# Kernel tuning notes

Measured on AMD Instinct MI355X. Metric: run time of the kernel, lower is better.

The kernel has to match this reference:

```python
import jax, jax.numpy as jnp
import numpy as np

E = 8      # num_experts
K = 2      # active_experts
D = 1024   # embed_size
H = 4 * D  # ffn hidden


def setup_inputs() -> dict:
    key = jax.random.key(0)
    ks = jax.random.split(key, 7)
    s_in = 1.0 / np.sqrt(D)
    s_h = 1.0 / np.sqrt(H)
    return {
        "x":  jax.random.normal(ks[0], (4, 2048, D), dtype=jnp.float32),
        "Wr": jax.random.uniform(ks[1], (D, E), jnp.float32, -s_in, s_in),
        "br": jax.random.uniform(ks[2], (E,), jnp.float32, -s_in, s_in),
        "W1": jax.random.uniform(ks[3], (E, D, H), jnp.float32, -s_in, s_in),
        "b1": jax.random.uniform(ks[4], (E, H), jnp.float32, -s_in, s_in),
        "W2": jax.random.uniform(ks[5], (E, H, D), jnp.float32, -s_h, s_h),
        "b2": jax.random.uniform(ks[6], (E, D), jnp.float32, -s_h, s_h),
    }


def reference(x, Wr, br, W1, b1, W2, b2):
    # Router: softmax over experts, top-k values, renormalize.
    logits = jnp.einsum("bsd,de->bse", x, Wr) + br            # [B,S,E]
    probs = jax.nn.softmax(logits, axis=-1)
    topk_vals, _ = jax.lax.top_k(probs, K)                     # [B,S,K]
    gates = topk_vals / topk_vals.sum(axis=-1, keepdims=True)  # [B,S,K]

    # Original bug (reproduced faithfully): the mask-multiply-sum is identity,
    # and slot index i selects experts[i], so only experts 0..K-1 run on ALL tokens.
    h = jax.nn.relu(jnp.einsum("bsd,kdh->bskh", x, W1[:K]) + b1[:K])  # [B,S,K,H]
    y = jnp.einsum("bskh,khd->bskd", h, W2[:K]) + b2[:K]               # [B,S,K,D]
    return jnp.einsum("bskd,bsk->bsd", y, gates)                       # [B,S,D]
```

## Files before the change

kernel.cpp:

```cpp
#include <hip/hip_runtime.h>
#include <hip/hip_bf16.h>

#define T_TOK 8192
#define DDIM  1024
#define HDIM  4096
#define KCAT  8192
#define NE    8

typedef __attribute__((ext_vector_type(8))) __bf16 bf16x8;
typedef __attribute__((ext_vector_type(4))) float  f32x4;

__device__ __forceinline__ unsigned short f2bf(float f) {
  union { float f; unsigned u; } v; v.f = f;
  unsigned r = v.u + 0x7fffu + ((v.u >> 16) & 1u);
  return (unsigned short)(r >> 16);
}

__device__ __forceinline__ void gl_lds16(const unsigned short* g, char* l) {
  __builtin_amdgcn_global_load_lds(
      (__attribute__((address_space(1))) const void*)g,
      (__attribute__((address_space(3))) void*)l,
      16, 0, 0);
}

__global__ __launch_bounds__(256) void k_router(
    const float* __restrict__ x, const float* __restrict__ Wr,
    const float* __restrict__ br, unsigned short* __restrict__ xb,
    float* __restrict__ gates)
{
  const int lane = threadIdx.x & 63;
  const int wv   = threadIdx.x >> 6;
  const int t    = blockIdx.x * 4 + wv;
  const float* xr = x + (size_t)t * DDIM;
  unsigned short* xo = xb + (size_t)t * DDIM;

  float acc[NE];
#pragma unroll
  for (int e = 0; e < NE; ++e) acc[e] = 0.f;

#pragma unroll
  for (int i = 0; i < 4; ++i) {
    float4 v = *(const float4*)(xr + i * 256 + lane * 4);
    ushort4 o;
    o.x = f2bf(v.x); o.y = f2bf(v.y); o.z = f2bf(v.z); o.w = f2bf(v.w);
    *(ushort4*)(xo + i * 256 + lane * 4) = o;
    float vs[4] = {v.x, v.y, v.z, v.w};
#pragma unroll
    for (int j = 0; j < 4; ++j) {
      const float4* wr = (const float4*)(Wr + (size_t)(i * 256 + lane * 4 + j) * NE);
      float4 w0 = wr[0], w1 = wr[1];
      acc[0] += vs[j] * w0.x; acc[1] += vs[j] * w0.y;
      acc[2] += vs[j] * w0.z; acc[3] += vs[j] * w0.w;
      acc[4] += vs[j] * w1.x; acc[5] += vs[j] * w1.y;
      acc[6] += vs[j] * w1.z; acc[7] += vs[j] * w1.w;
    }
  }
#pragma unroll
  for (int e = 0; e < NE; ++e) {
#pragma unroll
    for (int s = 32; s > 0; s >>= 1) acc[e] += __shfl_xor(acc[e], s, 64);
  }
  if (lane == 0) {
    float lg[NE];
#pragma unroll
    for (int e = 0; e < NE; ++e) lg[e] = acc[e] + br[e];
    int a1 = 0; float m1 = lg[0];
#pragma unroll
    for (int e = 1; e < NE; ++e) if (lg[e] > m1) { m1 = lg[e]; a1 = e; }
    float m2 = -3.4e38f;
#pragma unroll
    for (int e = 0; e < NE; ++e) if (e != a1 && lg[e] > m2) m2 = lg[e];
    float g0 = 1.f / (1.f + expf(m2 - m1));
    gates[t * 2 + 0] = g0;
    gates[t * 2 + 1] = 1.f - g0;
  }
}

__global__ __launch_bounds__(256) void k_transpose(
    const float* __restrict__ in, unsigned short* __restrict__ out,
    int R, int C, int S, size_t inz, size_t outz)
{
  __shared__ float tile[32][33];
  in  += (size_t)blockIdx.z * inz;
  out += (size_t)blockIdx.z * outz;
  const int c0 = blockIdx.x * 32, r0 = blockIdx.y * 32;
  const int tx = threadIdx.x & 31, ty = threadIdx.x >> 5;
#pragma unroll
  for (int i = 0; i < 32; i += 8)
    tile[ty + i][tx] = in[(size_t)(r0 + ty + i) * C + (c0 + tx)];
  __syncthreads();
#pragma unroll
  for (int i = 0; i < 32; i += 8)
    out[(size_t)(c0 + ty + i) * S + (r0 + tx)] = f2bf(tile[tx][ty + i]);
}

template<int NT, int MODE>
__global__ __launch_bounds__(512, 2) void k_gemm2(
    const unsigned short* __restrict__ A,
    const unsigned short* __restrict__ B,
    unsigned short* __restrict__ Hout,
    float* __restrict__ P0, float* __restrict__ P1,
    const float* __restrict__ bias,
    const float* __restrict__ gates,
    int KA, int KB)
{
  __shared__ __align__(16) char lds[2 * 32768];

  const int tid = threadIdx.x;
  const int l = tid & 63, g = (l >> 4), l15 = l & 15;
  const int w = tid >> 6;
  const int wm = w >> 2, wn = w & 3;

  int bmIdx, bnIdx, bzIdx;
  {
    int lin = ((blockIdx.z * gridDim.y) + blockIdx.y) * gridDim.x + blockIdx.x;
    int xcd = lin & 7, slot = (lin >> 3) & 31;
    if (MODE == 0) {
      int r = lin >> 8;
      bmIdx = r * 8 + (slot >> 2);
      bnIdx = xcd * 4 + (slot & 3);
      bzIdx = 0;
    } else {
      bzIdx = xcd & 1;
      bmIdx = (xcd >> 1) * 8 + (slot >> 2);
      bnIdx = slot & 3;
    }
  }
  const int bn = bnIdx * 256;
  const int bm = bmIdx * 256;
  const int koff = bzIdx * (NT * 32);

  const int srow = tid >> 2;
  const int sc = (tid & 3) ^ ((srow >> 1) & 3);
  const unsigned short* As = A + (size_t)(bm + srow) * KA + koff + sc * 8;
  const unsigned short* Bs = B + (size_t)(bn + srow) * KB + koff + sc * 8;

  auto stage = [&](int T, int reg) {
    const unsigned short* src = (reg ? Bs : As) + T * 32;
    size_t rstride = (size_t)128 * (reg ? KB : KA);
    char* dst = lds + ((T & 1) << 15) + (reg << 14) + tid * 16;
    gl_lds16(src, dst);
    gl_lds16(src + rstride, dst + 8192);
  };

  int aoff[2][4], boff[4];
#pragma unroll
  for (int mh = 0; mh < 2; ++mh)
#pragma unroll
    for (int mi = 0; mi < 4; ++mi) {
      int r = wm * 128 + mh * 64 + mi * 16 + l15;
      aoff[mh][mi] = r * 64 + ((g ^ ((r >> 1) & 3)) * 16);
    }
#pragma unroll
  for (int nj = 0; nj < 4; ++nj) {
    int r = wn * 64 + nj * 16 + l15;
    boff[nj] = r * 64 + ((g ^ ((r >> 1) & 3)) * 16);
  }

  f32x4 acc[8][4];
#pragma unroll
  for (int i = 0; i < 8; ++i)
#pragma unroll
    for (int j = 0; j < 4; ++j) acc[i][j] = (f32x4){0.f, 0.f, 0.f, 0.f};

  stage(0, 0); stage(0, 1);

#define MFMA16(AI, A0, A1, A2, A3)                                                     \
    acc[(AI)+0][0] = __builtin_amdgcn_mfma_f32_16x16x32_bf16(A0, vb0, acc[(AI)+0][0], 0,0,0); \
    acc[(AI)+0][1] = __builtin_amdgcn_mfma_f32_16x16x32_bf16(A0, vb1, acc[(AI)+0][1], 0,0,0); \
    acc[(AI)+0][2] = __builtin_amdgcn_mfma_f32_16x16x32_bf16(A0, vb2, acc[(AI)+0][2], 0,0,0); \
    acc[(AI)+0][3] = __builtin_amdgcn_mfma_f32_16x16x32_bf16(A0, vb3, acc[(AI)+0][3], 0,0,0); \
    acc[(AI)+1][0] = __builtin_amdgcn_mfma_f32_16x16x32_bf16(A1, vb0, acc[(AI)+1][0], 0,0,0); \
    acc[(AI)+1][1] = __builtin_amdgcn_mfma_f32_16x16x32_bf16(A1, vb1, acc[(AI)+1][1], 0,0,0); \
    acc[(AI)+1][2] = __builtin_amdgcn_mfma_f32_16x16x32_bf16(A1, vb2, acc[(AI)+1][2], 0,0,0); \
    acc[(AI)+1][3] = __builtin_amdgcn_mfma_f32_16x16x32_bf16(A1, vb3, acc[(AI)+1][3], 0,0,0); \
    acc[(AI)+2][0] = __builtin_amdgcn_mfma_f32_16x16x32_bf16(A2, vb0, acc[(AI)+2][0], 0,0,0); \
    acc[(AI)+2][1] = __builtin_amdgcn_mfma_f32_16x16x32_bf16(A2, vb1, acc[(AI)+2][1], 0,0,0); \
    acc[(AI)+2][2] = __builtin_amdgcn_mfma_f32_16x16x32_bf16(A2, vb2, acc[(AI)+2][2], 0,0,0); \
    acc[(AI)+2][3] = __builtin_amdgcn_mfma_f32_16x16x32_bf16(A2, vb3, acc[(AI)+2][3], 0,0,0); \
    acc[(AI)+3][0] = __builtin_amdgcn_mfma_f32_16x16x32_bf16(A3, vb0, acc[(AI)+3][0], 0,0,0); \
    acc[(AI)+3][1] = __builtin_amdgcn_mfma_f32_16x16x32_bf16(A3, vb1, acc[(AI)+3][1], 0,0,0); \
    acc[(AI)+3][2] = __builtin_amdgcn_mfma_f32_16x16x32_bf16(A3, vb2, acc[(AI)+3][2], 0,0,0); \
    acc[(AI)+3][3] = __builtin_amdgcn_mfma_f32_16x16x32_bf16(A3, vb3, acc[(AI)+3][3], 0,0,0);

#define MPH(BUF, STG) do {                                                     \
    asm volatile("s_waitcnt vmcnt(0)" ::: "memory");                           \
    __builtin_amdgcn_s_barrier();                                              \
    const char* Ar_ = lds + ((BUF) << 15);                                     \
    const char* Br_ = Ar_ + 16384;                                             \
    bf16x8 vb0 = *(const bf16x8*)(Br_ + boff[0]);                              \
    bf16x8 vb1 = *(const bf16x8*)(Br_ + boff[1]);                              \
    bf16x8 vb2 = *(const bf16x8*)(Br_ + boff[2]);                              \
    bf16x8 vb3 = *(const bf16x8*)(Br_ + boff[3]);                              \
    bf16x8 vc0 = *(const bf16x8*)(Ar_ + aoff[0][0]);                           \
    bf16x8 vc1 = *(const bf16x8*)(Ar_ + aoff[0][1]);                           \
    bf16x8 vc2 = *(const bf16x8*)(Ar_ + aoff[0][2]);                           \
    bf16x8 vc3 = *(const bf16x8*)(Ar_ + aoff[0][3]);                           \
    bf16x8 vn0 = *(const bf16x8*)(Ar_ + aoff[1][0]);                           \
    bf16x8 vn1 = *(const bf16x8*)(Ar_ + aoff[1][1]);                           \
    bf16x8 vn2 = *(const bf16x8*)(Ar_ + aoff[1][2]);                           \
    bf16x8 vn3 = *(const bf16x8*)(Ar_ + aoff[1][3]);                           \
    asm volatile("" ::: "memory");                                             \
    STG;                                                                       \
    __builtin_amdgcn_s_setprio(1);                                             \
    MFMA16(0, vc0, vc1, vc2, vc3)                                              \
    MFMA16(4, vn0, vn1, vn2, vn3)                                              \
    __builtin_amdgcn_s_setprio(0);                                             \
    __builtin_amdgcn_s_barrier();                                              \
  } while (0)

  for (int tt = 0; tt < NT / 2 - 1; ++tt) {
    int t2 = tt * 2;
    MPH(0, { stage(t2 + 1, 0); stage(t2 + 1, 1); });
    MPH(1, { stage(t2 + 2, 0); stage(t2 + 2, 1); });
  }
  MPH(0, { stage(NT - 1, 0); stage(NT - 1, 1); });
  MPH(1, ;);
#undef MPH
#undef MFMA16

  if constexpr (MODE == 0) {
    const int ge = bn >> 12;
    float bcol[4];
#pragma unroll
    for (int nj = 0; nj < 4; ++nj) bcol[nj] = bias[bn + wn * 64 + nj * 16 + l15];
#pragma unroll
    for (int mi = 0; mi < 8; ++mi) {
#pragma unroll
      for (int rr = 0; rr < 4; ++rr) {
        int row = bm + wm * 128 + mi * 16 + g * 4 + rr;
        float gate = gates[row * 2 + ge];
        size_t rb = (size_t)row * KCAT + bn + wn * 64 + l15;
#pragma unroll
        for (int nj = 0; nj < 4; ++nj) {
          float v = acc[mi][nj][rr] + bcol[nj];
          Hout[rb + nj * 16] = f2bf(fmaxf(v, 0.f) * gate);
        }
      }
    }
  } else {
    float* P = bzIdx ? P1 : P0;
#pragma unroll
    for (int mi = 0; mi < 8; ++mi) {
#pragma unroll
      for (int rr = 0; rr < 4; ++rr) {
        int row = bm + wm * 128 + mi * 16 + g * 4 + rr;
        size_t rb = (size_t)row * DDIM + bn + wn * 64 + l15;
#pragma unroll
        for (int nj = 0; nj < 4; ++nj) P[rb + nj * 16] = acc[mi][nj][rr];
      }
    }
  }
}

__global__ __launch_bounds__(256) void k_combine(
    const float* __restrict__ P1, const float* __restrict__ b2,
    const float* __restrict__ gates, float* __restrict__ O)
{
  size_t i = ((size_t)blockIdx.x * 256 + threadIdx.x) * 4;
  int row = (int)(i >> 10), d = (int)(i & 1023);
  float g0 = gates[row * 2], g1 = gates[row * 2 + 1];
  float4 p0 = *(const float4*)(O + i);
  float4 p1 = *(const float4*)(P1 + i);
  float4 ba = *(const float4*)(b2 + d);
  float4 bb = *(const float4*)(b2 + DDIM + d);
  float4 r;
  r.x = p0.x + p1.x + g0 * ba.x + g1 * bb.x;
  r.y = p0.y + p1.y + g0 * ba.y + g1 * bb.y;
  r.z = p0.z + p1.z + g0 * ba.z + g1 * bb.z;
  r.w = p0.w + p1.w + g0 * ba.w + g1 * bb.w;
  *(float4*)(O + i) = r;
}

extern "C" void kernel_launch(void* const* d_in, const int* in_sizes, int n_in,
                              void* d_out, int out_size, void* d_ws, size_t ws_size,
                              hipStream_t stream) {
  const float* x  = (const float*)d_in[0];
  const float* Wr = (const float*)d_in[1];
  const float* br = (const float*)d_in[2];
  const float* W1 = (const float*)d_in[3];
  const float* b1 = (const float*)d_in[4];
  const float* W2 = (const float*)d_in[5];
  const float* b2 = (const float*)d_in[6];

  char* ws = (char*)d_ws;
  unsigned short* xb    = (unsigned short*)(ws);
  unsigned short* W1T   = (unsigned short*)(ws + (16u << 20));
  unsigned short* W2T   = (unsigned short*)(ws + (32u << 20));
  float*          gates = (float*)(ws + (48u << 20));
  unsigned short* hbuf  = (unsigned short*)(ws + (49u << 20));
  float*          P1    = (float*)(ws);

  k_router<<<dim3(T_TOK / 4), dim3(256), 0, stream>>>(x, Wr, br, xb, gates);

  k_transpose<<<dim3(HDIM / 32, DDIM / 32, 2), dim3(256), 0, stream>>>(
      W1, W1T, DDIM, HDIM, DDIM, (size_t)DDIM * HDIM, (size_t)HDIM * DDIM);
  k_transpose<<<dim3(DDIM / 32, HDIM / 32, 2), dim3(256), 0, stream>>>(
      W2, W2T, HDIM, DDIM, KCAT, (size_t)HDIM * DDIM, (size_t)HDIM);

  k_gemm2<32, 0><<<dim3(KCAT / 256, T_TOK / 256, 1), dim3(512), 0, stream>>>(
      xb, W1T, hbuf, nullptr, nullptr, b1, gates, DDIM, DDIM);

  k_gemm2<128, 1><<<dim3(DDIM / 256, T_TOK / 256, 2), dim3(512), 0, stream>>>(
      hbuf, W2T, nullptr, (float*)d_out, P1, nullptr, nullptr, KCAT, KCAT);

  k_combine<<<dim3(T_TOK * DDIM / 4 / 256), dim3(256), 0, stream>>>(
      P1, b2, gates, (float*)d_out);
}
```

Baseline: 325.4 us.

## Software-pipeline LDS fragment reads with double register buffers in GEMM main loop

Restructures the GEMM main loop so that LDS fragment reads for the next k-tile go into a second register set while MFMAs consume the current one. This removes one barrier per phase and lets LDS read latency overlap with matrix math. The launch bound's min-blocks-per-CU hint is dropped, since the doubled fragment registers raise VGPR pressure, which may lower occupancy. A sched_barrier pins the instruction order.

Result: no change. 322.0 us (-1.0%).

```diff
diff --git a/kernel.cpp b/kernel.cpp
--- a/kernel.cpp
+++ b/kernel.cpp
@@ -95,7 +95,7 @@
 }
 
 template<int NT, int MODE>
-__global__ __launch_bounds__(512, 2) void k_gemm2(
+__global__ __launch_bounds__(512) void k_gemmp(
     const unsigned short* __restrict__ A,
     const unsigned short* __restrict__ B,
     unsigned short* __restrict__ Hout,
@@ -163,61 +163,88 @@
 #pragma unroll
     for (int j = 0; j < 4; ++j) acc[i][j] = (f32x4){0.f, 0.f, 0.f, 0.f};
 
-  stage(0, 0); stage(0, 1);
-
-#define MFMA16(AI, A0, A1, A2, A3)                                                     \
-    acc[(AI)+0][0] = __builtin_amdgcn_mfma_f32_16x16x32_bf16(A0, vb0, acc[(AI)+0][0], 0,0,0); \
-    acc[(AI)+0][1] = __builtin_amdgcn_mfma_f32_16x16x32_bf16(A0, vb1, acc[(AI)+0][1], 0,0,0); \
-    acc[(AI)+0][2] = __builtin_amdgcn_mfma_f32_16x16x32_bf16(A0, vb2, acc[(AI)+0][2], 0,0,0); \
-    acc[(AI)+0][3] = __builtin_amdgcn_mfma_f32_16x16x32_bf16(A0, vb3, acc[(AI)+0][3], 0,0,0); \
-    acc[(AI)+1][0] = __builtin_amdgcn_mfma_f32_16x16x32_bf16(A1, vb0, acc[(AI)+1][0], 0,0,0); \
-    acc[(AI)+1][1] = __builtin_amdgcn_mfma_f32_16x16x32_bf16(A1, vb1, acc[(AI)+1][1], 0,0,0); \
-    acc[(AI)+1][2] = __builtin_amdgcn_mfma_f32_16x16x32_bf16(A1, vb2, acc[(AI)+1][2], 0,0,0); \
-    acc[(AI)+1][3] = __builtin_amdgcn_mfma_f32_16x16x32_bf16(A1, vb3, acc[(AI)+1][3], 0,0,0); \
-    acc[(AI)+2][0] = __builtin_amdgcn_mfma_f32_16x16x32_bf16(A2, vb0, acc[(AI)+2][0], 0,0,0); \
-    acc[(AI)+2][1] = __builtin_amdgcn_mfma_f32_16x16x32_bf16(A2, vb1, acc[(AI)+2][1], 0,0,0); \
-    acc[(AI)+2][2] = __builtin_amdgcn_mfma_f32_16x16x32_bf16(A2, vb2, acc[(AI)+2][2], 0,0,0); \
-    acc[(AI)+2][3] = __builtin_amdgcn_mfma_f32_16x16x32_bf16(A2, vb3, acc[(AI)+2][3], 0,0,0); \
-    acc[(AI)+3][0] = __builtin_amdgcn_mfma_f32_16x16x32_bf16(A3, vb0, acc[(AI)+3][0], 0,0,0); \
-    acc[(AI)+3][1] = __builtin_amdgcn_mfma_f32_16x16x32_bf16(A3, vb1, acc[(AI)+3][1], 0,0,0); \
-    acc[(AI)+3][2] = __builtin_amdgcn_mfma_f32_16x16x32_bf16(A3, vb2, acc[(AI)+3][2], 0,0,0); \
-    acc[(AI)+3][3] = __builtin_amdgcn_mfma_f32_16x16x32_bf16(A3, vb3, acc[(AI)+3][3], 0,0,0);
-
-#define MPH(BUF, STG) do {                                                     \
+  bf16x8 RA[12], RB[12];
+
+#define READS(R, b) do {                                                       \
+    const char* Ar_ = lds + ((b) << 15);                                       \
+    const char* Br_ = Ar_ + 16384;                                             \
+    R[0]  = *(const bf16x8*)(Br_ + boff[0]);                                   \
+    R[1]  = *(const bf16x8*)(Br_ + boff[1]);                                   \
+    R[2]  = *(const bf16x8*)(Br_ + boff[2]);                                   \
+    R[3]  = *(const bf16x8*)(Br_ + boff[3]);                                   \
+    R[4]  = *(const bf16x8*)(Ar_ + aoff[0][0]);                                \
+    R[5]  = *(const bf16x8*)(Ar_ + aoff[0][1]);                                \
+    R[6]  = *(const bf16x8*)(Ar_ + aoff[0][2]);                                \
+    R[7]  = *(const bf16x8*)(Ar_ + aoff[0][3]);                                \
+    R[8]  = *(const bf16x8*)(Ar_ + aoff[1][0]);                                \
+    R[9]  = *(const bf16x8*)(Ar_ + aoff[1][1]);                                \
+    R[10] = *(const bf16x8*)(Ar_ + aoff[1][2]);                                \
+    R[11] = *(const bf16x8*)(Ar_ + aoff[1][3]);                                \
+  } while (0)
+
+#define MFMA32(R)                                                              \
+    acc[0][0] = __builtin_amdgcn_mfma_f32_16x16x32_bf16(R[4],  R[0], acc[0][0], 0,0,0); \
+    acc[0][1] = __builtin_amdgcn_mfma_f32_16x16x32_bf16(R[4],  R[1], acc[0][1], 0,0,0); \
+    acc[0][2] = __builtin_amdgcn_mfma_f32_16x16x32_bf16(R[4],  R[2], acc[0][2], 0,0,0); \
+    acc[0][3] = __builtin_amdgcn_mfma_f32_16x16x32_bf16(R[4],  R[3], acc[0][3], 0,0,0); \
+    acc[1][0] = __builtin_amdgcn_mfma_f32_16x16x32_bf16(R[5],  R[0], acc[1][0], 0,0,0); \
+    acc[1][1] = __builtin_amdgcn_mfma_f32_16x16x32_bf16(R[5],  R[1], acc[1][1], 0,0,0); \
+    acc[1][2] = __builtin_amdgcn_mfma_f32_16x16x32_bf16(R[5],  R[2], acc[1][2], 0,0,0); \
+    acc[1][3] = __builtin_amdgcn_mfma_f32_16x16x32_bf16(R[5],  R[3], acc[1][3], 0,0,0); \
+    acc[2][0] = __builtin_amdgcn_mfma_f32_16x16x32_bf16(R[6],  R[0], acc[2][0], 0,0,0); \
+    acc[2][1] = __builtin_amdgcn_mfma_f32_16x16x32_bf16(R[6],  R[1], acc[2][1], 0,0,0); \
+    acc[2][2] = __builtin_amdgcn_mfma_f32_16x16x32_bf16(R[6],  R[2], acc[2][2], 0,0,0); \
+    acc[2][3] = __builtin_amdgcn_mfma_f32_16x16x32_bf16(R[6],  R[3], acc[2][3], 0,0,0); \
+    acc[3][0] = __builtin_amdgcn_mfma_f32_16x16x32_bf16(R[7],  R[0], acc[3][0], 0,0,0); \
+    acc[3][1] = __builtin_amdgcn_mfma_f32_16x16x32_bf16(R[7],  R[1], acc[3][1], 0,0,0); \
+    acc[3][2] = __builtin_amdgcn_mfma_f32_16x16x32_bf16(R[7],  R[2], acc[3][2], 0,0,0); \
+    acc[3][3] = __builtin_amdgcn_mfma_f32_16x16x32_bf16(R[7],  R[3], acc[3][3], 0,0,0); \
+    acc[4][0] = __builtin_amdgcn_mfma_f32_16x16x32_bf16(R[8],  R[0], acc[4][0], 0,0,0); \
+    acc[4][1] = __builtin_amdgcn_mfma_f32_16x16x32_bf16(R[8],  R[1], acc[4][1], 0,0,0); \
+    acc[4][2] = __builtin_amdgcn_mfma_f32_16x16x32_bf16(R[8],  R[2], acc[4][2], 0,0,0); \
+    acc[4][3] = __builtin_amdgcn_mfma_f32_16x16x32_bf16(R[8],  R[3], acc[4][3], 0,0,0); \
+    acc[5][0] = __builtin_amdgcn_mfma_f32_16x16x32_bf16(R[9],  R[0], acc[5][0], 0,0,0); \
+    acc[5][1] = __builtin_amdgcn_mfma_f32_16x16x32_bf16(R[9],  R[1], acc[5][1], 0,0,0); \
+    acc[5][2] = __builtin_amdgcn_mfma_f32_16x16x32_bf16(R[9],  R[2], acc[5][2], 0,0,0); \
+    acc[5][3] = __builtin_amdgcn_mfma_f32_16x16x32_bf16(R[9],  R[3], acc[5][3], 0,0,0); \
+    acc[6][0] = __builtin_amdgcn_mfma_f32_16x16x32_bf16(R[10], R[0], acc[6][0], 0,0,0); \
+    acc[6][1] = __builtin_amdgcn_mfma_f32_16x16x32_bf16(R[10], R[1], acc[6][1], 0,0,0); \
+    acc[6][2] = __builtin_amdgcn_mfma_f32_16x16x32_bf16(R[10], R[2], acc[6][2], 0,0,0); \
+    acc[6][3] = __builtin_amdgcn_mfma_f32_16x16x32_bf16(R[10], R[3], acc[6][3], 0,0,0); \
+    acc[7][0] = __builtin_amdgcn_mfma_f32_16x16x32_bf16(R[11], R[0], acc[7][0], 0,0,0); \
+    acc[7][1] = __builtin_amdgcn_mfma_f32_16x16x32_bf16(R[11], R[1], acc[7][1], 0,0,0); \
+    acc[7][2] = __builtin_amdgcn_mfma_f32_16x16x32_bf16(R[11], R[2], acc[7][2], 0,0,0); \
+    acc[7][3] = __builtin_amdgcn_mfma_f32_16x16x32_bf16(R[11], R[3], acc[7][3], 0,0,0);
+
+#define PH(RD, RDB, MF, DOSTG, STGT) do {                                      \
     asm volatile("s_waitcnt vmcnt(0)" ::: "memory");                           \
     __builtin_amdgcn_s_barrier();                                              \
-    const char* Ar_ = lds + ((BUF) << 15);                                     \
-    const char* Br_ = Ar_ + 16384;                                             \
-    bf16x8 vb0 = *(const bf16x8*)(Br_ + boff[0]);                              \
-    bf16x8 vb1 = *(const bf16x8*)(Br_ + boff[1]);                              \
-    bf16x8 vb2 = *(const bf16x8*)(Br_ + boff[2]);                              \
-    bf16x8 vb3 = *(const bf16x8*)(Br_ + boff[3]);                              \
-    bf16x8 vc0 = *(const bf16x8*)(Ar_ + aoff[0][0]);                           \
-    bf16x8 vc1 = *(const bf16x8*)(Ar_ + aoff[0][1]);                           \
-    bf16x8 vc2 = *(const bf16x8*)(Ar_ + aoff[0][2]);                           \
-    bf16x8 vc3 = *(const bf16x8*)(Ar_ + aoff[0][3]);                           \
-    bf16x8 vn0 = *(const bf16x8*)(Ar_ + aoff[1][0]);                           \
-    bf16x8 vn1 = *(const bf16x8*)(Ar_ + aoff[1][1]);                           \
-    bf16x8 vn2 = *(const bf16x8*)(Ar_ + aoff[1][2]);                           \
-    bf16x8 vn3 = *(const bf16x8*)(Ar_ + aoff[1][3]);                           \
+    READS(RD, RDB);                                                            \
+    if (DOSTG) { stage((STGT), 0); stage((STGT), 1); }                         \
     asm volatile("" ::: "memory");                                             \
-    STG;                                                                       \
+    __builtin_amdgcn_sched_barrier(0);                                         \
     __builtin_amdgcn_s_setprio(1);                                             \
-    MFMA16(0, vc0, vc1, vc2, vc3)                                              \
-    MFMA16(4, vn0, vn1, vn2, vn3)                                              \
+    MFMA32(MF)                                                                 \
     __builtin_amdgcn_s_setprio(0);                                             \
-    __builtin_amdgcn_s_barrier();                                              \
   } while (0)
 
+  stage(0, 0); stage(0, 1);
+  asm volatile("s_waitcnt vmcnt(0)" ::: "memory");
+  __builtin_amdgcn_s_barrier();
+  READS(RA, 0);
+  stage(1, 0); stage(1, 1);
+
   for (int tt = 0; tt < NT / 2 - 1; ++tt) {
-    int t2 = tt * 2;
-    MPH(0, { stage(t2 + 1, 0); stage(t2 + 1, 1); });
-    MPH(1, { stage(t2 + 2, 0); stage(t2 + 2, 1); });
-  }
-  MPH(0, { stage(NT - 1, 0); stage(NT - 1, 1); });
-  MPH(1, ;);
-#undef MPH
-#undef MFMA16
+    PH(RB, 1, RA, true, 2 * tt + 2);
+    PH(RA, 0, RB, true, 2 * tt + 3);
+  }
+  PH(RB, 1, RA, false, 0);
+  __builtin_amdgcn_s_setprio(1);
+  MFMA32(RB)
+  __builtin_amdgcn_s_setprio(0);
+#undef PH
+#undef MFMA32
+#undef READS
 
   if constexpr (MODE == 0) {
     const int ge = bn >> 12;
@@ -298,10 +325,10 @@
   k_transpose<<<dim3(DDIM / 32, HDIM / 32, 2), dim3(256), 0, stream>>>(
       W2, W2T, HDIM, DDIM, KCAT, (size_t)HDIM * DDIM, (size_t)HDIM);
 
-  k_gemm2<32, 0><<<dim3(KCAT / 256, T_TOK / 256, 1), dim3(512), 0, stream>>>(
+  k_gemmp<32, 0><<<dim3(KCAT / 256, T_TOK / 256, 1), dim3(512), 0, stream>>>(
       xb, W1T, hbuf, nullptr, nullptr, b1, gates, DDIM, DDIM);
 
-  k_gemm2<128, 1><<<dim3(DDIM / 256, T_TOK / 256, 2), dim3(512), 0, stream>>>(
+  k_gemmp<128, 1><<<dim3(DDIM / 256, T_TOK / 256, 2), dim3(512), 0, stream>>>(
       hbuf, W2T, nullptr, (float*)d_out, P1, nullptr, nullptr, KCAT, KCAT);
 
   k_combine<<<dim3(T_TOK * DDIM / 4 / 256), dim3(256), 0, stream>>>(
```
